# Performance work log

Hardware: AMD Instinct MI355X
Metric: run time of the kernel (lower is better)

## Reference

```python
import jax, jax.numpy as jnp
import numpy as np

# Metadata layout (matches init_kwargs): 3 keys x [bid p/v x5 levels, ask p/v x5 levels]
N_KEYS, N_LEVELS, FEATS_PER_KEY = 3, 5, 20
_base = np.arange(N_KEYS)[:, None] * FEATS_PER_KEY      # [K,1]
_lvl = np.arange(N_LEVELS)[None, :] * 2                  # [1,L] price stride 2 (price,volume interleave)
BID_IDX = jnp.asarray(_base + _lvl)                      # [K,L] bid price column indices
ASK_IDX = jnp.asarray(_base + 10 + _lvl)                 # [K,L] ask price column indices


def setup_inputs() -> dict:
    key = jax.random.key(0)
    predictions = jax.random.normal(key, (64, 8192, 60), dtype=jnp.float32)
    return {"predictions": predictions}


def reference(predictions):
    # Gather bid/ask price levels for all keys at once: [B, S, K, L]
    bid = predictions[:, :, BID_IDX]
    ask = predictions[:, :, ASK_IDX]
    # Original sums, over every key / timestep / adjacent-level pair, the BATCH MEAN of
    # relu violations; that equals mean over batch then sum over (S, K, level-pairs).
    ask_viol = jnp.maximum(ask[..., :-1] - ask[..., 1:], 0.0)   # ask_k > ask_{k+1} violation
    bid_viol = jnp.maximum(bid[..., 1:] - bid[..., :-1], 0.0)   # bid_{k+1} > bid_k violation
    spread_viol = jnp.maximum(bid[..., 0] - ask[..., 0], 0.0)   # bid_1 > ask_1 violation
    total = (ask_viol.mean(axis=0).sum()
             + bid_viol.mean(axis=0).sum()
             + spread_viol.mean(axis=0).sum())
    return total
```

## Files before the change

### kernel.cpp

```cpp
#include <hip/hip_runtime.h>


__global__ __launch_bounds__(256) void structural_loss_kernel(
    const float* __restrict__ pred, float* __restrict__ out, int nrows) {
    int r = blockIdx.x * blockDim.x + threadIdx.x;

    float s = 0.0f;
    if (r < nrows) {
        const float4* rp = reinterpret_cast<const float4*>(pred + (size_t)r * 60);
        float p[60];
#pragma unroll
        for (int j = 0; j < 15; ++j) {
            float4 v = rp[j];
            p[4 * j + 0] = v.x;
            p[4 * j + 1] = v.y;
            p[4 * j + 2] = v.z;
            p[4 * j + 3] = v.w;
        }
#pragma unroll
        for (int k = 0; k < 3; ++k) {
            const float* q = p + k * 20;
#pragma unroll
            for (int l = 0; l < 4; ++l) {
                float av = q[10 + 2 * l] - q[12 + 2 * l];
                float bv = q[2 * l + 2] - q[2 * l];
                s += fmaxf(av, 0.0f) + fmaxf(bv, 0.0f);
            }
            s += fmaxf(q[0] - q[10], 0.0f);
        }
    }

#pragma unroll
    for (int off = 32; off > 0; off >>= 1)
        s += __shfl_down(s, off, 64);

    __shared__ float wsum[4];
    int lane = threadIdx.x & 63;
    int wid = threadIdx.x >> 6;
    if (lane == 0) wsum[wid] = s;
    __syncthreads();
    if (threadIdx.x == 0) {
        float t = (wsum[0] + wsum[1] + wsum[2] + wsum[3]) * (1.0f / 64.0f);
        atomicAdd(out, t);
    }
}

extern "C" void kernel_launch(void* const* d_in, const int* in_sizes, int n_in,
                              void* d_out, int out_size, void* d_ws, size_t ws_size,
                              hipStream_t stream) {
    const float* pred = (const float*)d_in[0];
    float* out = (float*)d_out;

    int nrows = in_sizes[0] / 60;
    int block = 256;
    int grid = (nrows + block - 1) / block;

    hipMemsetAsync(out, 0, sizeof(float), stream);
    structural_loss_kernel<<<grid, block, 0, stream>>>(pred, out, nrows);
}
```

Before: 179.6 us.

## Process float4 chunks per thread with coalesced grid-stride loads and two-pass reduction

Each thread now handles one float4 of the flat input per grid-stride step instead of a whole 60-float row, so a wavefront's loads are contiguous and fully coalesced rather than strided by 240 bytes. Per-chunk sign masks derived from the chunk index modulo 5 select which ask, bid and spread comparisons apply, using two extra scalar loads from neighbouring chunks. The memset and atomicAdd are replaced by per-block partial sums in workspace plus a single-block final reduction kernel, at the cost of a second launch and redundant neighbour loads that should mostly hit cache.

```diff
diff --git a/kernel.cpp b/kernel.cpp
--- a/kernel.cpp
+++ b/kernel.cpp
@@ -1,48 +1,50 @@
 #include <hip/hip_runtime.h>
 
 
-__global__ __launch_bounds__(256) void structural_loss_kernel(
-    const float* __restrict__ pred, float* __restrict__ out, int nrows) {
-    int r = blockIdx.x * blockDim.x + threadIdx.x;
+__global__ __launch_bounds__(256) void sl_partial(
+    const float4* __restrict__ p4, const float* __restrict__ p,
+    float* __restrict__ partial, unsigned nf4) {
+    unsigned gid = blockIdx.x * 256u + threadIdx.x;
+    unsigned stride = gridDim.x * 256u;
 
     float s = 0.0f;
-    if (r < nrows) {
-        const float4* rp = reinterpret_cast<const float4*>(pred + (size_t)r * 60);
-        float p[60];
-#pragma unroll
-        for (int j = 0; j < 15; ++j) {
-            float4 v = rp[j];
-            p[4 * j + 0] = v.x;
-            p[4 * j + 1] = v.y;
-            p[4 * j + 2] = v.z;
-            p[4 * j + 3] = v.w;
-        }
-#pragma unroll
-        for (int k = 0; k < 3; ++k) {
-            const float* q = p + k * 20;
-#pragma unroll
-            for (int l = 0; l < 4; ++l) {
-                float av = q[10 + 2 * l] - q[12 + 2 * l];
-                float bv = q[2 * l + 2] - q[2 * l];
-                s += fmaxf(av, 0.0f) + fmaxf(bv, 0.0f);
-            }
-            s += fmaxf(q[0] - q[10], 0.0f);
-        }
+    for (unsigned f = gid; f < nf4; f += stride) {
+        float4 a = p4[f];
+        unsigned fn = f + 1u; if (fn >= nf4) fn = nf4 - 1u;
+        unsigned f2 = f + 2u; if (f2 >= nf4) f2 = nf4 - 1u;
+        float n0 = p[(size_t)fn * 4u];
+        float z2 = p[(size_t)f2 * 4u + 2u];
+
+        unsigned c = f % 5u;
+        float dA = (c < 2u) ? 1.0f : ((c == 2u) ? 0.0f : -1.0f);
+        float dB = (c < 2u) ? 1.0f : ((c == 4u) ? 0.0f : -1.0f);
+        float sS = (c == 0u) ? 1.0f : 0.0f;
+
+        s += fmaxf(dA * (a.z - a.x), 0.0f);
+        s += fmaxf(dB * (n0 - a.z), 0.0f);
+        s += fmaxf(sS * (a.x - z2), 0.0f);
     }
 
 #pragma unroll
-    for (int off = 32; off > 0; off >>= 1)
-        s += __shfl_down(s, off, 64);
+    for (int off = 32; off > 0; off >>= 1) s += __shfl_down(s, off, 64);
+    __shared__ float ws[4];
+    if ((threadIdx.x & 63u) == 0u) ws[threadIdx.x >> 6] = s;
+    __syncthreads();
+    if (threadIdx.x == 0)
+        partial[blockIdx.x] = ws[0] + ws[1] + ws[2] + ws[3];
+}
 
-    __shared__ float wsum[4];
-    int lane = threadIdx.x & 63;
-    int wid = threadIdx.x >> 6;
-    if (lane == 0) wsum[wid] = s;
+__global__ __launch_bounds__(256) void sl_final(
+    const float* __restrict__ partial, float* __restrict__ out, int n) {
+    float s = 0.0f;
+    for (int i = threadIdx.x; i < n; i += 256) s += partial[i];
+#pragma unroll
+    for (int off = 32; off > 0; off >>= 1) s += __shfl_down(s, off, 64);
+    __shared__ float ws[4];
+    if ((threadIdx.x & 63u) == 0u) ws[threadIdx.x >> 6] = s;
     __syncthreads();
-    if (threadIdx.x == 0) {
-        float t = (wsum[0] + wsum[1] + wsum[2] + wsum[3]) * (1.0f / 64.0f);
-        atomicAdd(out, t);
-    }
+    if (threadIdx.x == 0)
+        out[0] = (ws[0] + ws[1] + ws[2] + ws[3]) * (1.0f / 64.0f);
 }
 
 extern "C" void kernel_launch(void* const* d_in, const int* in_sizes, int n_in,
@@ -50,11 +52,12 @@
                               hipStream_t stream) {
     const float* pred = (const float*)d_in[0];
     float* out = (float*)d_out;
+    float* partial = (float*)d_ws;
 
-    int nrows = in_sizes[0] / 60;
-    int block = 256;
-    int grid = (nrows + block - 1) / block;
+    unsigned nf4 = (unsigned)(in_sizes[0] / 4);
+    int grid = 2048;
 
-    hipMemsetAsync(out, 0, sizeof(float), stream);
-    structural_loss_kernel<<<grid, block, 0, stream>>>(pred, out, nrows);
+    sl_partial<<<grid, 256, 0, stream>>>(
+        (const float4*)pred, pred, partial, nf4);
+    sl_final<<<1, 256, 0, stream>>>(partial, out, grid);
 }
```

Measured after the change: 177.6 us. About the same (-1.1%).
